# Kernel optimization log

Measured on AMD Instinct MI355X. Metric: run time of the kernel, lower is better.

The kernel has to match this reference:

```python
import jax, jax.numpy as jnp
import numpy as np

B, T, C_IN, CH, NRC, ED, NL, K = 16, 4096, 165, 256, 32, 64, 4, 512


def conv1x1(x, w, b):
    # x: [B,T,Cin], w: [Cout,Cin], b: [Cout]  (kernel-size-1 Conv1d == per-timestep matmul)
    return jnp.einsum('btc,oc->bto', x, w) + b


def resblock(x, wa, ba, wb, bb):
    h = jax.nn.relu(x)
    h = jax.nn.relu(conv1x1(h, wa, ba))
    h = conv1x1(h, wb, bb)
    return x + h


def quantize_level(res, embed):
    # res: [B,T,D], embed: [D,K]
    D = res.shape[-1]
    flat = res.reshape(-1, D)  # [N,D]
    dist = (flat * flat).sum(1, keepdims=True) - 2.0 * (flat @ embed) + (embed * embed).sum(0, keepdims=True)  # [N,K]
    ind = jnp.argmin(dist, axis=1)
    q = jnp.take(embed.T, ind, axis=0).reshape(res.shape)  # codebook gather
    diff = jnp.mean(jnp.square(jax.lax.stop_gradient(q) - res))
    q_st = res + jax.lax.stop_gradient(q - res)  # straight-through
    return q_st, diff


def _p(key, shape, fan_in):
    return jax.random.normal(key, shape, dtype=jnp.float32) / np.sqrt(fan_in)


def setup_inputs() -> dict:
    key = jax.random.key(0)
    ks = jax.random.split(key, 32)
    d = {
        'x': jax.random.normal(ks[0], (B, T, C_IN), dtype=jnp.float32),
        'enc_w1': _p(ks[1], (CH // 2, C_IN), C_IN), 'enc_b1': jnp.zeros((CH // 2,), jnp.float32),
        'enc_w2': _p(ks[2], (CH, CH // 2), CH // 2), 'enc_b2': jnp.zeros((CH,), jnp.float32),
        'enc_w3': _p(ks[3], (CH, CH), CH), 'enc_b3': jnp.zeros((CH,), jnp.float32),
        'enc_res_wa': _p(ks[4], (2, NRC, CH), CH), 'enc_res_ba': jnp.zeros((2, NRC), jnp.float32),
        'enc_res_wb': _p(ks[5], (2, CH, NRC), NRC), 'enc_res_bb': jnp.zeros((2, CH), jnp.float32),
        # quantize_conv: Conv(256->64)
        'q_w': _p(ks[6], (ED, CH), CH), 'q_b': jnp.zeros((ED,), jnp.float32),
        # 4 codebooks [D,K] (torch.randn init)
        'embeds': jax.random.normal(ks[7], (NL, ED, K), dtype=jnp.float32),
        'dec_w1': _p(ks[8], (CH, ED), ED), 'dec_b1': jnp.zeros((CH,), jnp.float32),
        'dec_res_wa': _p(ks[9], (2, NRC, CH), CH), 'dec_res_ba': jnp.zeros((2, NRC), jnp.float32),
        'dec_res_wb': _p(ks[10], (2, CH, NRC), NRC), 'dec_res_bb': jnp.zeros((2, CH), jnp.float32),
        'dec_w2': _p(ks[11], (CH // 2, CH), CH), 'dec_b2': jnp.zeros((CH // 2,), jnp.float32),
        'dec_w3': _p(ks[12], (C_IN, CH // 2), CH // 2), 'dec_b3': jnp.zeros((C_IN,), jnp.float32),
    }
    return d


def reference(x, enc_w1, enc_b1, enc_w2, enc_b2, enc_w3, enc_b3,
              enc_res_wa, enc_res_ba, enc_res_wb, enc_res_bb,
              q_w, q_b, embeds,
              dec_w1, dec_b1, dec_res_wa, dec_res_ba, dec_res_wb, dec_res_bb,
              dec_w2, dec_b2, dec_w3, dec_b3):
    # work entirely in [B,T,C] layout (transposes in the torch code cancel)
    h = jax.nn.relu(conv1x1(x, enc_w1, enc_b1))
    h = jax.nn.relu(conv1x1(h, enc_w2, enc_b2))
    h = conv1x1(h, enc_w3, enc_b3)
    for i in range(2):
        h = resblock(h, enc_res_wa[i], enc_res_ba[i], enc_res_wb[i], enc_res_bb[i])
    h = jax.nn.relu(h)
    quant = conv1x1(h, q_w, q_b)  # [B,T,64]

    residual = quant
    diffs = []
    main_q = None
    for i in range(NL):
        q, d = quantize_level(residual, embeds[i])
        diffs.append(d)
        residual = residual - q
        if i == 0:
            main_q = q
    diff = jnp.mean(jnp.stack(diffs))[None]  # shape [1]

    d = conv1x1(main_q, dec_w1, dec_b1)
    for i in range(2):
        d = resblock(d, dec_res_wa[i], dec_res_ba[i], dec_res_wb[i], dec_res_bb[i])
    d = jax.nn.relu(d)
    d = jax.nn.relu(conv1x1(d, dec_w2, dec_b2))
    d = conv1x1(d, dec_w3, dec_b3)  # [B,T,165]
    return d, diff
```

## Files before the change

kernel.cpp:

```cpp
#include <hip/hip_runtime.h>

#define NROWS 65536
#define SB 256

__device__ __forceinline__ float frelu(float v) { return fmaxf(v, 0.f); }

#define OFF_WT1   0
#define OFF_WT2   21504
#define OFF_WT3   54272
#define OFF_WTQ   119808
#define OFF_WTD1  136192
#define OFF_WTD2  152576
#define OFF_WTD3  185344
#define OFF_WAPE  218112
#define OFF_WBTE  234496
#define OFF_WAPD  250880
#define OFF_WBTD  267264
#define OFF_ETG   283648
#define OFF_EN2   414720
#define OFF_DSUM  416768
#define PREP_N    416769

__global__ void prep_k(const float* __restrict__ ew1, const float* __restrict__ ew2,
                       const float* __restrict__ ew3, const float* __restrict__ qw,
                       const float* __restrict__ dw1, const float* __restrict__ dw2,
                       const float* __restrict__ dw3, const float* __restrict__ ewa,
                       const float* __restrict__ ewb, const float* __restrict__ dwa,
                       const float* __restrict__ dwb, const float* __restrict__ embeds,
                       float* __restrict__ W) {
  int idx = blockIdx.x * 256 + threadIdx.x;
  if (idx < 21504) {
    int k = idx >> 7, o = idx & 127;
    W[OFF_WT1 + idx] = (k < 165) ? ew1[o * 165 + k] : 0.f;
    return;
  }
  idx -= 21504;
  if (idx < 32768) {
    int k = idx >> 8, o = idx & 255;
    W[OFF_WT2 + idx] = ew2[o * 128 + k];
    return;
  }
  idx -= 32768;
  if (idx < 65536) {
    int k = idx >> 8, o = idx & 255;
    W[OFF_WT3 + idx] = ew3[o * 256 + k];
    return;
  }
  idx -= 65536;
  if (idx < 16384) {
    int k = idx >> 6, o = idx & 63;
    W[OFF_WTQ + idx] = qw[o * 256 + k];
    return;
  }
  idx -= 16384;
  if (idx < 16384) {
    int k = idx >> 8, o = idx & 255;
    W[OFF_WTD1 + idx] = dw1[o * 64 + k];
    return;
  }
  idx -= 16384;
  if (idx < 32768) {
    int k = idx >> 7, o = idx & 127;
    W[OFF_WTD2 + idx] = dw2[o * 256 + k];
    return;
  }
  idx -= 32768;
  if (idx < 32768) {
    int k = idx >> 8, o = idx & 255;
    W[OFF_WTD3 + idx] = (o < 165) ? dw3[o * 128 + k] : 0.f;
    return;
  }
  idx -= 32768;
  if (idx < 16384) {
    int l = idx >> 13, rem = idx & 8191;
    int k4 = rem >> 7, rem2 = rem & 127, o = rem2 >> 2, kk = rem2 & 3;
    W[OFF_WAPE + idx] = ewa[l * 8192 + o * 256 + k4 * 4 + kk];
    return;
  }
  idx -= 16384;
  if (idx < 16384) {
    int l = idx >> 13, rem = idx & 8191;
    int k = rem >> 8, o = rem & 255;
    W[OFF_WBTE + idx] = ewb[l * 8192 + o * 32 + k];
    return;
  }
  idx -= 16384;
  if (idx < 16384) {
    int l = idx >> 13, rem = idx & 8191;
    int k4 = rem >> 7, rem2 = rem & 127, o = rem2 >> 2, kk = rem2 & 3;
    W[OFF_WAPD + idx] = dwa[l * 8192 + o * 256 + k4 * 4 + kk];
    return;
  }
  idx -= 16384;
  if (idx < 16384) {
    int l = idx >> 13, rem = idx & 8191;
    int k = rem >> 8, o = rem & 255;
    W[OFF_WBTD + idx] = dwb[l * 8192 + o * 32 + k];
    return;
  }
  idx -= 16384;
  if (idx < 131072) {
    int d = idx & 63, k = (idx >> 6) & 511, l = idx >> 15;
    W[OFF_ETG + idx] = embeds[(l * 64 + d) * 512 + k];
    return;
  }
  idx -= 131072;
  if (idx < 2048) {
    int l = idx >> 9, k = idx & 511;
    float s = 0.f;
    for (int d = 0; d < 64; ++d) {
      float e = embeds[(l * 64 + d) * 512 + k];
      s = fmaf(e, e, s);
    }
    W[OFF_EN2 + idx] = s;
    return;
  }
  idx -= 2048;
  if (idx == 0) W[OFF_DSUM] = 0.f;
}

template <int CIN, int CINP, int COUT, int CP, int INSTRIDE, int OUTSTRIDE, bool RELU_IN,
          bool RELU_OUT>
__global__ __launch_bounds__(256, 4) void conv2_k(const float* in, const float* __restrict__ wT,
                                                  const float* __restrict__ b, float* out) {
  constexpr int COUTP = 64 * CP;
  constexpr bool GUARD = (COUT != COUTP);
  typedef float vCP __attribute__((ext_vector_type(CP)));
  __shared__ float xs[32][CINP];
  const int tid = threadIdx.x, lane = tid & 63, wv = tid >> 6;
  const long row0 = (long)blockIdx.x * 32;

  for (int i = tid; i < 32 * CINP; i += 256) {
    const int r = i / CINP, c = i % CINP;
    float v = (CIN == CINP || c < CIN) ? in[(row0 + r) * (long)INSTRIDE + c] : 0.f;
    if (RELU_IN) v = frelu(v);
    xs[r][c] = v;
  }
  __syncthreads();

  float acc[8][CP];
#pragma unroll
  for (int i = 0; i < 8; ++i)
#pragma unroll
    for (int j = 0; j < CP; ++j) acc[i][j] = 0.f;

  const float* wbase = wT + lane * CP;
#pragma unroll 4
  for (int k0 = 0; k0 < CINP; k0 += 4) {
    vCP wk[4];
#pragma unroll
    for (int kk = 0; kk < 4; ++kk) wk[kk] = *(const vCP*)(wbase + (k0 + kk) * COUTP);
#pragma unroll
    for (int rj = 0; rj < 8; ++rj) {
      const float4 x = *(const float4*)(&xs[wv * 8 + rj][k0]);
#pragma unroll
      for (int j = 0; j < CP; ++j) {
        acc[rj][j] = fmaf(x.x, wk[0][j], acc[rj][j]);
        acc[rj][j] = fmaf(x.y, wk[1][j], acc[rj][j]);
        acc[rj][j] = fmaf(x.z, wk[2][j], acc[rj][j]);
        acc[rj][j] = fmaf(x.w, wk[3][j], acc[rj][j]);
      }
    }
  }

  float bias[CP];
#pragma unroll
  for (int j = 0; j < CP; ++j) {
    const int o = lane * CP + j;
    bias[j] = (!GUARD || o < COUT) ? b[o] : 0.f;
  }
#pragma unroll
  for (int rj = 0; rj < 8; ++rj) {
    const long rbase = (row0 + wv * 8 + rj) * (long)OUTSTRIDE;
    if constexpr (!GUARD) {
      vCP v;
#pragma unroll
      for (int j = 0; j < CP; ++j) {
        const float t = acc[rj][j] + bias[j];
        v[j] = RELU_OUT ? frelu(t) : t;
      }
      *(vCP*)(out + rbase + lane * CP) = v;
    } else {
#pragma unroll
      for (int j = 0; j < CP; ++j) {
        const int o = lane * CP + j;
        if (o < COUT) {
          const float t = acc[rj][j] + bias[j];
          out[rbase + o] = RELU_OUT ? frelu(t) : t;
        }
      }
    }
  }
}

template <int CIN, int COUT, int COUTP, int INSTRIDE, int OUTSTRIDE, bool RELU_IN, bool RELU_OUT>
__global__ __launch_bounds__(512, 2) void conv6_k(const float* __restrict__ in,
                                                  const float* __restrict__ wT,
                                                  const float* __restrict__ b,
                                                  float* __restrict__ out) {
  constexpr int MAXD = (CIN > COUT) ? CIN : COUT;
  __shared__ float lds[MAXD * 65];
  const int tid = threadIdx.x;
  const int lane = tid & 63;
  const int wv = __builtin_amdgcn_readfirstlane(tid >> 6);
  const long row0 = (long)blockIdx.x * 64;

  constexpr int C4 = CIN / 4;
  for (int i = tid; i < 64 * C4; i += 512) {
    const int r = i / C4, c4 = i % C4;
    float4 v = *(const float4*)(in + (row0 + r) * (long)INSTRIDE + c4 * 4);
    if (RELU_IN) {
      v.x = frelu(v.x);
      v.y = frelu(v.y);
      v.z = frelu(v.z);
      v.w = frelu(v.w);
    }
    lds[(c4 * 4 + 0) * 65 + r] = v.x;
    lds[(c4 * 4 + 1) * 65 + r] = v.y;
    lds[(c4 * 4 + 2) * 65 + r] = v.z;
    lds[(c4 * 4 + 3) * 65 + r] = v.w;
  }
  __syncthreads();

  float acc[32];
#pragma unroll
  for (int j = 0; j < 32; ++j) acc[j] = 0.f;

  const float* wrow = wT + wv * 32;
#pragma unroll 2
  for (int k = 0; k < CIN; ++k) {
    const float xv = lds[k * 65 + lane];
    const float* wk = wrow + (long)k * COUTP;
#pragma unroll
    for (int j = 0; j < 32; ++j) acc[j] = fmaf(xv, wk[j], acc[j]);
  }

  const float* bb = b + wv * 32;
#pragma unroll
  for (int j = 0; j < 32; ++j) {
    float t = acc[j] + bb[j];
    acc[j] = RELU_OUT ? frelu(t) : t;
  }

  __syncthreads();
#pragma unroll
  for (int j = 0; j < 32; ++j) lds[(wv * 32 + j) * 65 + lane] = acc[j];
  __syncthreads();

  constexpr int O4 = COUT / 4;
  for (int i = tid; i < 64 * O4; i += 512) {
    const int r = i / O4, c4 = i % O4;
    float4 v;
    v.x = lds[(c4 * 4 + 0) * 65 + r];
    v.y = lds[(c4 * 4 + 1) * 65 + r];
    v.z = lds[(c4 * 4 + 2) * 65 + r];
    v.w = lds[(c4 * 4 + 3) * 65 + r];
    *(float4*)(out + (row0 + r) * (long)OUTSTRIDE + c4 * 4) = v;
  }
}

__global__ __launch_bounds__(512, 4) void resblock_pair_k(
    float* xbuf, const float* __restrict__ waP, const float* __restrict__ ba,
    const float* __restrict__ wbT, const float* __restrict__ bb) {
  __shared__ float wls[8192];
  __shared__ float ts[64][36];
  const int tid = threadIdx.x, lane = tid & 63, wv = tid >> 6;
  const long row0 = (long)blockIdx.x * 64;
  const int o32 = lane & 31, rh = lane >> 5;

  for (int li = 0; li < 2; ++li) {
    __syncthreads();
    for (int i = tid; i < 8192; i += 512) wls[i] = waP[li * 8192 + i];
    __syncthreads();

    {
      float a0 = 0.f, a1 = 0.f, a2 = 0.f, a3 = 0.f;
      const float* xrow = xbuf + (row0 + wv * 8 + rh * 4) * (long)SB;
#pragma unroll 4
      for (int k0 = 0; k0 < 256; k0 += 4) {
        const float4 wq = *(const float4*)(&wls[k0 * 32 + o32 * 4]);
        const float4 x0 = *(const float4*)(xrow + 0 * SB + k0);
        const float4 x1 = *(const float4*)(xrow + 1 * SB + k0);
        const float4 x2 = *(const float4*)(xrow + 2 * SB + k0);
        const float4 x3 = *(const float4*)(xrow + 3 * SB + k0);
        a0 = fmaf(frelu(x0.x), wq.x, a0);
        a0 = fmaf(frelu(x0.y), wq.y, a0);
        a0 = fmaf(frelu(x0.z), wq.z, a0);
        a0 = fmaf(frelu(x0.w), wq.w, a0);
        a1 = fmaf(frelu(x1.x), wq.x, a1);
        a1 = fmaf(frelu(x1.y), wq.y, a1);
        a1 = fmaf(frelu(x1.z), wq.z, a1);
        a1 = fmaf(frelu(x1.w), wq.w, a1);
        a2 = fmaf(frelu(x2.x), wq.x, a2);
        a2 = fmaf(frelu(x2.y), wq.y, a2);
        a2 = fmaf(frelu(x2.z), wq.z, a2);
        a2 = fmaf(frelu(x2.w), wq.w, a2);
        a3 = fmaf(frelu(x3.x), wq.x, a3);
        a3 = fmaf(frelu(x3.y), wq.y, a3);
        a3 = fmaf(frelu(x3.z), wq.z, a3);
        a3 = fmaf(frelu(x3.w), wq.w, a3);
      }
      const float bal = ba[li * 32 + o32];
      const int rB = wv * 8 + rh * 4;
      ts[rB + 0][o32] = frelu(a0 + bal);
      ts[rB + 1][o32] = frelu(a1 + bal);
      ts[rB + 2][o32] = frelu(a2 + bal);
      ts[rB + 3][o32] = frelu(a3 + bal);
    }

    __syncthreads();
    for (int i = tid; i < 8192; i += 512) wls[i] = wbT[li * 8192 + i];
    __syncthreads();

    float acc2[8][4];
#pragma unroll
    for (int i = 0; i < 8; ++i)
#pragma unroll
      for (int j = 0; j < 4; ++j) acc2[i][j] = 0.f;

#pragma unroll
    for (int k0 = 0; k0 < 32; k0 += 4) {
      const float4 wk0 = *(const float4*)(&wls[(k0 + 0) * 256 + lane * 4]);
      const float4 wk1 = *(const float4*)(&wls[(k0 + 1) * 256 + lane * 4]);
      const float4 wk2 = *(const float4*)(&wls[(k0 + 2) * 256 + lane * 4]);
      const float4 wk3 = *(const float4*)(&wls[(k0 + 3) * 256 + lane * 4]);
#pragma unroll
      for (int rj = 0; rj < 8; ++rj) {
        const float4 t4 = *(const float4*)(&ts[wv * 8 + rj][k0]);
        acc2[rj][0] = fmaf(t4.x, wk0.x, acc2[rj][0]);
        acc2[rj][1] = fmaf(t4.x, wk0.y, acc2[rj][1]);
        acc2[rj][2] = fmaf(t4.x, wk0.z, acc2[rj][2]);
        acc2[rj][3] = fmaf(t4.x, wk0.w, acc2[rj][3]);
        acc2[rj][0] = fmaf(t4.y, wk1.x, acc2[rj][0]);
        acc2[rj][1] = fmaf(t4.y, wk1.y, acc2[rj][1]);
        acc2[rj][2] = fmaf(t4.y, wk1.z, acc2[rj][2]);
        acc2[rj][3] = fmaf(t4.y, wk1.w, acc2[rj][3]);
        acc2[rj][0] = fmaf(t4.z, wk2.x, acc2[rj][0]);
        acc2[rj][1] = fmaf(t4.z, wk2.y, acc2[rj][1]);
        acc2[rj][2] = fmaf(t4.z, wk2.z, acc2[rj][2]);
        acc2[rj][3] = fmaf(t4.z, wk2.w, acc2[rj][3]);
        acc2[rj][0] = fmaf(t4.w, wk3.x, acc2[rj][0]);
        acc2[rj][1] = fmaf(t4.w, wk3.y, acc2[rj][1]);
        acc2[rj][2] = fmaf(t4.w, wk3.z, acc2[rj][2]);
        acc2[rj][3] = fmaf(t4.w, wk3.w, acc2[rj][3]);
      }
    }
    const float4 bbv = *(const float4*)(bb + li * 256 + lane * 4);
#pragma unroll
    for (int rj = 0; rj < 8; ++rj) {
      float* xp = xbuf + (row0 + wv * 8 + rj) * (long)SB + lane * 4;
      const float4 xv = *(const float4*)xp;
      float4 nv;
      nv.x = xv.x + acc2[rj][0] + bbv.x;
      nv.y = xv.y + acc2[rj][1] + bbv.y;
      nv.z = xv.z + acc2[rj][2] + bbv.z;
      nv.w = xv.w + acc2[rj][3] + bbv.w;
      *(float4*)xp = nv;
    }
  }
}

__global__ __launch_bounds__(256, 4) void vq_k(float* buf, const float* __restrict__ embeds,
                                               const float* __restrict__ en2,
                                               const float* __restrict__ etg,
                                               float* __restrict__ dsum) {
  __shared__ float resL[32][68];
  const int tid = threadIdx.x;
  const int lane = tid & 63;
  const int wv = tid >> 6;
  const long row0 = (long)blockIdx.x * 32;

  for (int rj = 0; rj < 8; ++rj) {
    const int r = wv * 8 + rj;
    resL[r][lane] = buf[(row0 + r) * (long)SB + lane];
  }

  float dloc = 0.f;

  for (int l = 0; l < 4; ++l) {
    float best[8];
    int bk[8];
#pragma unroll
    for (int i = 0; i < 8; ++i) {
      best[i] = 3.4e38f;
      bk[i] = 0;
    }

    for (int kc = 0; kc < 2; ++kc) {
      float acc[8][4];
#pragma unroll
      for (int i = 0; i < 8; ++i)
#pragma unroll
        for (int j = 0; j < 4; ++j) acc[i][j] = 0.f;

      const float* eb = embeds + ((long)l << 15) + (kc << 8) + lane * 4;
#pragma unroll 2
      for (int dq = 0; dq < 16; ++dq) {
        float4 x4[8];
#pragma unroll
        for (int rj = 0; rj < 8; ++rj) x4[rj] = *(const float4*)(&resL[wv * 8 + rj][dq * 4]);
#pragma unroll
        for (int dd = 0; dd < 4; ++dd) {
          const float4 e4 = *(const float4*)(eb + ((dq * 4 + dd) << 9));
#pragma unroll
          for (int rj = 0; rj < 8; ++rj) {
            const float xv = dd == 0 ? x4[rj].x : dd == 1 ? x4[rj].y : dd == 2 ? x4[rj].z : x4[rj].w;
            acc[rj][0] = fmaf(xv, e4.x, acc[rj][0]);
            acc[rj][1] = fmaf(xv, e4.y, acc[rj][1]);
            acc[rj][2] = fmaf(xv, e4.z, acc[rj][2]);
            acc[rj][3] = fmaf(xv, e4.w, acc[rj][3]);
          }
        }
      }

      const float4 e2 = *(const float4*)(en2 + l * 512 + kc * 256 + lane * 4);
#pragma unroll
      for (int rj = 0; rj < 8; ++rj) {
#pragma unroll
        for (int j = 0; j < 4; ++j) {
          const float ev = j == 0 ? e2.x : j == 1 ? e2.y : j == 2 ? e2.z : e2.w;
          const float s = fmaf(-2.f, acc[rj][j], ev);
          const int k = kc * 256 + lane * 4 + j;
          if (s < best[rj]) {
            best[rj] = s;
            bk[rj] = k;
          }
        }
      }
    }

#pragma unroll
    for (int rj = 0; rj < 8; ++rj) {
      float bv = best[rj];
      int bi = bk[rj];
#pragma unroll
      for (int m = 1; m < 64; m <<= 1) {
        const float ov = __shfl_xor(bv, m, 64);
        const int ok = __shfl_xor(bi, m, 64);
        if (ov < bv || (ov == bv && ok < bi)) {
          bv = ov;
          bi = ok;
        }
      }
      bk[rj] = bi;
    }

#pragma unroll
    for (int rj = 0; rj < 8; ++rj) {
      const int r = wv * 8 + rj;
      const float q = etg[((long)((l << 9) + bk[rj])) * 64 + lane];
      const float res = resL[r][lane];
      const float t = q - res;
      const float qst = res + t;
      dloc = fmaf(t, t, dloc);
      resL[r][lane] = res - qst;
      if (l == 0) buf[(row0 + r) * (long)SB + lane] = qst;
    }
  }

#pragma unroll
  for (int m = 1; m < 64; m <<= 1) dloc += __shfl_xor(dloc, m, 64);
  if (lane == 0) atomicAdd(dsum, dloc);
}

__global__ void finalize_k(const float* __restrict__ dsum, float* __restrict__ out) {
  if (threadIdx.x == 0 && blockIdx.x == 0)
    out[0] = *dsum * (1.0f / (4.0f * 65536.0f * 64.0f));
}

extern "C" void kernel_launch(void* const* d_in, const int* in_sizes, int n_in, void* d_out,
                              int out_size, void* d_ws, size_t ws_size, hipStream_t stream) {
  (void)in_sizes; (void)n_in; (void)out_size; (void)ws_size;
  const float* x = (const float*)d_in[0];
  const float* enc_w1 = (const float*)d_in[1];
  const float* enc_b1 = (const float*)d_in[2];
  const float* enc_w2 = (const float*)d_in[3];
  const float* enc_b2 = (const float*)d_in[4];
  const float* enc_w3 = (const float*)d_in[5];
  const float* enc_b3 = (const float*)d_in[6];
  const float* enc_res_wa = (const float*)d_in[7];
  const float* enc_res_ba = (const float*)d_in[8];
  const float* enc_res_wb = (const float*)d_in[9];
  const float* enc_res_bb = (const float*)d_in[10];
  const float* q_w = (const float*)d_in[11];
  const float* q_b = (const float*)d_in[12];
  const float* embeds = (const float*)d_in[13];
  const float* dec_w1 = (const float*)d_in[14];
  const float* dec_b1 = (const float*)d_in[15];
  const float* dec_res_wa = (const float*)d_in[16];
  const float* dec_res_ba = (const float*)d_in[17];
  const float* dec_res_wb = (const float*)d_in[18];
  const float* dec_res_bb = (const float*)d_in[19];
  const float* dec_w2 = (const float*)d_in[20];
  const float* dec_b2 = (const float*)d_in[21];
  const float* dec_w3 = (const float*)d_in[22];
  const float* dec_b3 = (const float*)d_in[23];

  float* ws = (float*)d_ws;
  float* buf = ws;
  float* W = ws + (long)NROWS * SB;

  float* dout = (float*)d_out;

  prep_k<<<(PREP_N + 255) / 256, 256, 0, stream>>>(enc_w1, enc_w2, enc_w3, q_w, dec_w1, dec_w2,
                                                   dec_w3, enc_res_wa, enc_res_wb, dec_res_wa,
                                                   dec_res_wb, embeds, W);

  const int GB = NROWS / 32;
  const int GR = NROWS / 64;

  conv2_k<165, 168, 128, 2, 165, SB, false, true><<<GB, 256, 0, stream>>>(x, W + OFF_WT1, enc_b1, buf);
  conv2_k<128, 128, 256, 4, SB, SB, false, true><<<GB, 256, 0, stream>>>(buf, W + OFF_WT2, enc_b2, buf);
  conv6_k<256, 256, 256, SB, SB, false, false><<<GR, 512, 0, stream>>>(buf, W + OFF_WT3, enc_b3, buf);
  resblock_pair_k<<<GR, 512, 0, stream>>>(buf, W + OFF_WAPE, enc_res_ba, W + OFF_WBTE, enc_res_bb);
  conv2_k<256, 256, 64, 1, SB, SB, true, false><<<GB, 256, 0, stream>>>(buf, W + OFF_WTQ, q_b, buf);

  vq_k<<<GB, 256, 0, stream>>>(buf, embeds, W + OFF_EN2, W + OFF_ETG, W + OFF_DSUM);

  conv2_k<64, 64, 256, 4, SB, SB, false, false><<<GB, 256, 0, stream>>>(buf, W + OFF_WTD1, dec_b1, buf);
  resblock_pair_k<<<GR, 512, 0, stream>>>(buf, W + OFF_WAPD, dec_res_ba, W + OFF_WBTD, dec_res_bb);
  conv2_k<256, 256, 128, 2, SB, SB, true, true><<<GB, 256, 0, stream>>>(buf, W + OFF_WTD2, dec_b2, buf);
  conv2_k<128, 128, 165, 4, SB, 165, false, false><<<GB, 256, 0, stream>>>(buf, W + OFF_WTD3, dec_b3, dout);

  finalize_k<<<1, 64, 0, stream>>>(W + OFF_DSUM, dout + (long)NROWS * 165);
}
```

Baseline: 1.222 ms.

## Fuse quantize conv, VQ and decoder first conv; fuse last two decoder convs

The quantize 1x1 conv, the 4-level residual VQ and the first decoder conv now run in one kernel that keeps the intermediates in shared memory. The final two decoder convs are fused the same way, and the encoder's second conv switches to the conv6 kernel variant. This removes several global-memory round trips of the 65536x256 activation buffer and a few kernel launches. In exchange the fused kernels use more shared memory (about 49 KB) and have lower launch_bounds occupancy.

Result: faster. 1.171 ms (-4.2%).

```diff
diff --git a/kernel.cpp b/kernel.cpp
--- a/kernel.cpp
+++ b/kernel.cpp
@@ -360,19 +360,47 @@
   }
 }
 
-__global__ __launch_bounds__(256, 4) void vq_k(float* buf, const float* __restrict__ embeds,
-                                               const float* __restrict__ en2,
-                                               const float* __restrict__ etg,
-                                               float* __restrict__ dsum) {
+__global__ __launch_bounds__(256, 3) void vq_fused_k(
+    float* buf, const float* __restrict__ wTq, const float* __restrict__ qb,
+    const float* __restrict__ embeds, const float* __restrict__ en2,
+    const float* __restrict__ etg, float* __restrict__ dsum,
+    const float* __restrict__ wTd1, const float* __restrict__ d1b) {
+  __shared__ float xs[32][256];
   __shared__ float resL[32][68];
+  __shared__ float mq[32][68];
   const int tid = threadIdx.x;
   const int lane = tid & 63;
   const int wv = tid >> 6;
   const long row0 = (long)blockIdx.x * 32;
 
-  for (int rj = 0; rj < 8; ++rj) {
-    const int r = wv * 8 + rj;
-    resL[r][lane] = buf[(row0 + r) * (long)SB + lane];
+  for (int i = tid; i < 32 * 256; i += 256) {
+    const int r = i >> 8, c = i & 255;
+    xs[r][c] = frelu(buf[(row0 + r) * (long)SB + c]);
+  }
+  __syncthreads();
+
+  {
+    float qacc[8];
+#pragma unroll
+    for (int i = 0; i < 8; ++i) qacc[i] = 0.f;
+#pragma unroll 2
+    for (int k0 = 0; k0 < 256; k0 += 4) {
+      const float w0 = wTq[(k0 + 0) * 64 + lane];
+      const float w1 = wTq[(k0 + 1) * 64 + lane];
+      const float w2 = wTq[(k0 + 2) * 64 + lane];
+      const float w3 = wTq[(k0 + 3) * 64 + lane];
+#pragma unroll
+      for (int rj = 0; rj < 8; ++rj) {
+        const float4 x = *(const float4*)(&xs[wv * 8 + rj][k0]);
+        qacc[rj] = fmaf(x.x, w0, qacc[rj]);
+        qacc[rj] = fmaf(x.y, w1, qacc[rj]);
+        qacc[rj] = fmaf(x.z, w2, qacc[rj]);
+        qacc[rj] = fmaf(x.w, w3, qacc[rj]);
+      }
+    }
+    const float qbv = qb[lane];
+#pragma unroll
+    for (int rj = 0; rj < 8; ++rj) resL[wv * 8 + rj][lane] = qacc[rj] + qbv;
   }
 
   float dloc = 0.f;
@@ -454,13 +482,159 @@
       const float qst = res + t;
       dloc = fmaf(t, t, dloc);
       resL[r][lane] = res - qst;
-      if (l == 0) buf[(row0 + r) * (long)SB + lane] = qst;
+      if (l == 0) mq[r][lane] = qst;
     }
   }
 
 #pragma unroll
   for (int m = 1; m < 64; m <<= 1) dloc += __shfl_xor(dloc, m, 64);
   if (lane == 0) atomicAdd(dsum, dloc);
+
+  {
+    float acc1[8][4];
+#pragma unroll
+    for (int i = 0; i < 8; ++i)
+#pragma unroll
+      for (int j = 0; j < 4; ++j) acc1[i][j] = 0.f;
+
+    const float* w1base = wTd1 + lane * 4;
+#pragma unroll 2
+    for (int d = 0; d < 64; d += 2) {
+      const float4 wA = *(const float4*)(w1base + (d + 0) * 256);
+      const float4 wB = *(const float4*)(w1base + (d + 1) * 256);
+#pragma unroll
+      for (int rj = 0; rj < 8; ++rj) {
+        const int r = wv * 8 + rj;
+        const float xA = mq[r][d];
+        const float xB = mq[r][d + 1];
+        acc1[rj][0] = fmaf(xA, wA.x, acc1[rj][0]);
+        acc1[rj][1] = fmaf(xA, wA.y, acc1[rj][1]);
+        acc1[rj][2] = fmaf(xA, wA.z, acc1[rj][2]);
+        acc1[rj][3] = fmaf(xA, wA.w, acc1[rj][3]);
+        acc1[rj][0] = fmaf(xB, wB.x, acc1[rj][0]);
+        acc1[rj][1] = fmaf(xB, wB.y, acc1[rj][1]);
+        acc1[rj][2] = fmaf(xB, wB.z, acc1[rj][2]);
+        acc1[rj][3] = fmaf(xB, wB.w, acc1[rj][3]);
+      }
+    }
+    const float4 bv = *(const float4*)(d1b + lane * 4);
+#pragma unroll
+    for (int rj = 0; rj < 8; ++rj) {
+      float4 v;
+      v.x = acc1[rj][0] + bv.x;
+      v.y = acc1[rj][1] + bv.y;
+      v.z = acc1[rj][2] + bv.z;
+      v.w = acc1[rj][3] + bv.w;
+      *(float4*)(buf + (row0 + wv * 8 + rj) * (long)SB + lane * 4) = v;
+    }
+  }
+}
+
+__global__ __launch_bounds__(256, 3) void dec23_k(const float* __restrict__ in,
+                                                  const float* __restrict__ wTd2,
+                                                  const float* __restrict__ b2,
+                                                  const float* __restrict__ wTd3,
+                                                  const float* __restrict__ b3,
+                                                  float* __restrict__ out) {
+  __shared__ float xs[32][256];
+  __shared__ float ts[32][132];
+  const int tid = threadIdx.x, lane = tid & 63, wv = tid >> 6;
+  const long row0 = (long)blockIdx.x * 32;
+
+  for (int i = tid; i < 32 * 256; i += 256) {
+    const int r = i >> 8, c = i & 255;
+    xs[r][c] = frelu(in[(row0 + r) * (long)SB + c]);
+  }
+  __syncthreads();
+
+  {
+    float a2[8][2];
+#pragma unroll
+    for (int i = 0; i < 8; ++i) {
+      a2[i][0] = 0.f;
+      a2[i][1] = 0.f;
+    }
+    const float* w2base = wTd2 + lane * 2;
+#pragma unroll 2
+    for (int k0 = 0; k0 < 256; k0 += 4) {
+      const float2 w0 = *(const float2*)(w2base + (k0 + 0) * 128);
+      const float2 w1 = *(const float2*)(w2base + (k0 + 1) * 128);
+      const float2 w2v = *(const float2*)(w2base + (k0 + 2) * 128);
+      const float2 w3 = *(const float2*)(w2base + (k0 + 3) * 128);
+#pragma unroll
+      for (int rj = 0; rj < 8; ++rj) {
+        const float4 x = *(const float4*)(&xs[wv * 8 + rj][k0]);
+        a2[rj][0] = fmaf(x.x, w0.x, a2[rj][0]);
+        a2[rj][1] = fmaf(x.x, w0.y, a2[rj][1]);
+        a2[rj][0] = fmaf(x.y, w1.x, a2[rj][0]);
+        a2[rj][1] = fmaf(x.y, w1.y, a2[rj][1]);
+        a2[rj][0] = fmaf(x.z, w2v.x, a2[rj][0]);
+        a2[rj][1] = fmaf(x.z, w2v.y, a2[rj][1]);
+        a2[rj][0] = fmaf(x.w, w3.x, a2[rj][0]);
+        a2[rj][1] = fmaf(x.w, w3.y, a2[rj][1]);
+      }
+    }
+    const float b20 = b2[lane * 2 + 0];
+    const float b21 = b2[lane * 2 + 1];
+#pragma unroll
+    for (int rj = 0; rj < 8; ++rj) {
+      const int r = wv * 8 + rj;
+      ts[r][lane * 2 + 0] = frelu(a2[rj][0] + b20);
+      ts[r][lane * 2 + 1] = frelu(a2[rj][1] + b21);
+    }
+  }
+
+  {
+    float a3[8][4];
+#pragma unroll
+    for (int i = 0; i < 8; ++i)
+#pragma unroll
+      for (int j = 0; j < 4; ++j) a3[i][j] = 0.f;
+
+    const float* w3base = wTd3 + lane * 4;
+#pragma unroll 2
+    for (int k0 = 0; k0 < 128; k0 += 4) {
+      const float4 wk0 = *(const float4*)(w3base + (k0 + 0) * 256);
+      const float4 wk1 = *(const float4*)(w3base + (k0 + 1) * 256);
+      const float4 wk2 = *(const float4*)(w3base + (k0 + 2) * 256);
+      const float4 wk3 = *(const float4*)(w3base + (k0 + 3) * 256);
+#pragma unroll
+      for (int rj = 0; rj < 8; ++rj) {
+        const float4 t4 = *(const float4*)(&ts[wv * 8 + rj][k0]);
+        a3[rj][0] = fmaf(t4.x, wk0.x, a3[rj][0]);
+        a3[rj][1] = fmaf(t4.x, wk0.y, a3[rj][1]);
+        a3[rj][2] = fmaf(t4.x, wk0.z, a3[rj][2]);
+        a3[rj][3] = fmaf(t4.x, wk0.w, a3[rj][3]);
+        a3[rj][0] = fmaf(t4.y, wk1.x, a3[rj][0]);
+        a3[rj][1] = fmaf(t4.y, wk1.y, a3[rj][1]);
+        a3[rj][2] = fmaf(t4.y, wk1.z, a3[rj][2]);
+        a3[rj][3] = fmaf(t4.y, wk1.w, a3[rj][3]);
+        a3[rj][0] = fmaf(t4.z, wk2.x, a3[rj][0]);
+        a3[rj][1] = fmaf(t4.z, wk2.y, a3[rj][1]);
+        a3[rj][2] = fmaf(t4.z, wk2.z, a3[rj][2]);
+        a3[rj][3] = fmaf(t4.z, wk2.w, a3[rj][3]);
+        a3[rj][0] = fmaf(t4.w, wk3.x, a3[rj][0]);
+        a3[rj][1] = fmaf(t4.w, wk3.y, a3[rj][1]);
+        a3[rj][2] = fmaf(t4.w, wk3.z, a3[rj][2]);
+        a3[rj][3] = fmaf(t4.w, wk3.w, a3[rj][3]);
+      }
+    }
+    float bias[4];
+#pragma unroll
+    for (int j = 0; j < 4; ++j) {
+      const int o = lane * 4 + j;
+      bias[j] = (o < 165) ? b3[o] : 0.f;
+    }
+#pragma unroll
+    for (int rj = 0; rj < 8; ++rj) {
+      const long rbase = (row0 + wv * 8 + rj) * 165L;
+#pragma unroll
+      for (int j = 0; j < 4; ++j) {
+        const int o = lane * 4 + j;
+        if (o < 165) out[rbase + o] = a3[rj][j] + bias[j];
+      }
+    }
+  }
 }
 
 __global__ void finalize_k(const float* __restrict__ dsum, float* __restrict__ out) {
@@ -510,17 +684,15 @@
   const int GR = NROWS / 64;
 
   conv2_k<165, 168, 128, 2, 165, SB, false, true><<<GB, 256, 0, stream>>>(x, W + OFF_WT1, enc_b1, buf);
-  conv2_k<128, 128, 256, 4, SB, SB, false, true><<<GB, 256, 0, stream>>>(buf, W + OFF_WT2, enc_b2, buf);
+  conv6_k<128, 256, 256, SB, SB, false, true><<<GR, 512, 0, stream>>>(buf, W + OFF_WT2, enc_b2, buf);
   conv6_k<256, 256, 256, SB, SB, false, false><<<GR, 512, 0, stream>>>(buf, W + OFF_WT3, enc_b3, buf);
   resblock_pair_k<<<GR, 512, 0, stream>>>(buf, W + OFF_WAPE, enc_res_ba, W + OFF_WBTE, enc_res_bb);
-  conv2_k<256, 256, 64, 1, SB, SB, true, false><<<GB, 256, 0, stream>>>(buf, W + OFF_WTQ, q_b, buf);
-
-  vq_k<<<GB, 256, 0, stream>>>(buf, embeds, W + OFF_EN2, W + OFF_ETG, W + OFF_DSUM);
-
-  conv2_k<64, 64, 256, 4, SB, SB, false, false><<<GB, 256, 0, stream>>>(buf, W + OFF_WTD1, dec_b1, buf);
+
+  vq_fused_k<<<GB, 256, 0, stream>>>(buf, W + OFF_WTQ, q_b, embeds, W + OFF_EN2, W + OFF_ETG,
+                                     W + OFF_DSUM, W + OFF_WTD1, dec_b1);
+
   resblock_pair_k<<<GR, 512, 0, stream>>>(buf, W + OFF_WAPD, dec_res_ba, W + OFF_WBTD, dec_res_bb);
-  conv2_k<256, 256, 128, 2, SB, SB, true, true><<<GB, 256, 0, stream>>>(buf, W + OFF_WTD2, dec_b2, buf);
-  conv2_k<128, 128, 165, 4, SB, 165, false, false><<<GB, 256, 0, stream>>>(buf, W + OFF_WTD3, dec_b3, dout);
+  dec23_k<<<GB, 256, 0, stream>>>(buf, W + OFF_WTD2, dec_b2, W + OFF_WTD3, dec_b3, dout);
 
   finalize_k<<<1, 64, 0, stream>>>(W + OFF_DSUM, dout + (long)NROWS * 165);
 }
```
